# Optimization experiments

Hardware: AMD Instinct MI355X
Metric: run time of the kernel (lower is better)

## Reference

```python
import jax, jax.numpy as jnp
import numpy as np

MARGIN = 1.0


def setup_inputs() -> dict:
    key = jax.random.key(0)
    k1, k2 = jax.random.split(key)
    N, D, C = 8192, 128, 64
    embeddings = jax.random.normal(k1, (N, D), dtype=jnp.float32)
    labels = jax.random.randint(k2, (N,), 0, C, dtype=jnp.int64)
    return {"embeddings": embeddings, "labels": labels}


def _pairwise_euclidean(x):
    # ||xi - xj|| via Gram trick; safe sqrt (zero grad at 0, matches masked use)
    sq = jnp.sum(x * x, axis=1)                      # [N]
    d2 = sq[:, None] + sq[None, :] - 2.0 * (x @ x.T)  # [N, N]
    d2 = jnp.maximum(d2, 0.0)
    pos = d2 > 0.0
    return jnp.where(pos, jnp.sqrt(jnp.where(pos, d2, 1.0)), 0.0)


def reference(embeddings, labels):
    N = embeddings.shape[0]
    dist = _pairwise_euclidean(embeddings)            # [N, N]
    same = labels[:, None] == labels[None, :]         # [N, N]
    eye = jnp.eye(N, dtype=bool)
    pos_mask = same & ~eye
    neg_mask = ~same

    neg_inf = jnp.float32(-jnp.inf)
    pos_inf = jnp.float32(jnp.inf)
    hardest_pos = jnp.max(jnp.where(pos_mask, dist, neg_inf), axis=1)  # [N]
    hardest_neg = jnp.min(jnp.where(neg_mask, dist, pos_inf), axis=1)  # [N]

    has_pos = jnp.any(pos_mask, axis=1)
    has_neg = jnp.any(neg_mask, axis=1)
    tl = jax.nn.relu(hardest_pos - hardest_neg + MARGIN)               # [N]
    valid = has_pos & has_neg & (tl > 0.0)

    total = jnp.sum(jnp.where(valid, tl, 0.0))
    count = jnp.sum(valid)
    return jnp.where(count > 0, total / jnp.maximum(count, 1).astype(total.dtype), jnp.float32(0.0))
```

## Files before the change

### kernel.cpp

```cpp
#include <hip/hip_runtime.h>
#include <math.h>

#define NN 8192
#define DD 128
#define BM 256
#define BN 64
#define NPART 16
#define JRANGE (NN / NPART)
#define NTILES (JRANGE / BN)

typedef __attribute__((ext_vector_type(4))) int i32x4;

#define WS_SJC 0
#define WS_HPK (NN * 16)
#define WS_HNK (WS_HPK + NN * 4)
#define WS_AH  (WS_HNK + NN * 4)
#define WS_AL  (WS_AH + NN * DD)

__device__ __forceinline__ unsigned fkey(float f) {
    unsigned u = __float_as_uint(f);
    return (u & 0x80000000u) ? ~u : (u | 0x80000000u);
}
__device__ __forceinline__ float fkey_inv(unsigned k) {
    unsigned u = (k & 0x80000000u) ? (k ^ 0x80000000u) : ~k;
    return __uint_as_float(u);
}

__global__ __launch_bounds__(256)
void prepq_k(const float* __restrict__ emb, const int* __restrict__ lab,
             float4* __restrict__ sjc, unsigned* __restrict__ hpK,
             unsigned* __restrict__ hnK, int* __restrict__ aH, int* __restrict__ aL) {
    const int lane = threadIdx.x & 63;
    const int w    = threadIdx.x >> 6;
    const int half = lane >> 5;
    const int l32  = lane & 31;
    const int row  = blockIdx.x * 8 + w * 2 + half;

    float4 v = reinterpret_cast<const float4*>(emb)[row * 32 + l32];
    float s = 0.f, m = 0.f;
    s = fmaf(v.x, v.x, s); m = fmaxf(m, fabsf(v.x));
    s = fmaf(v.y, v.y, s); m = fmaxf(m, fabsf(v.y));
    s = fmaf(v.z, v.z, s); m = fmaxf(m, fabsf(v.z));
    s = fmaf(v.w, v.w, s); m = fmaxf(m, fabsf(v.w));
#pragma unroll
    for (int off = 1; off < 32; off <<= 1) {
        s += __shfl_xor(s, off, 64);
        m = fmaxf(m, __shfl_xor(m, off, 64));
    }
    m = fmaxf(m, 1e-30f);
    float sA  = m * (1.0f / 127.0f);
    float inv = 127.0f / m;
    int h = 0, l = 0;
#define QSTEP(X, K) { \
        float a = rintf((X) * inv); \
        a = fminf(fmaxf(a, -127.f), 127.f); \
        float r = fmaf(-a, sA, (X)); \
        float b = rintf(r * inv * 256.0f); \
        b = fminf(fmaxf(b, -127.f), 127.f); \
        h |= ((int)a & 255) << (8 * (K)); \
        l |= ((int)b & 255) << (8 * (K)); }
    QSTEP(v.x, 0) QSTEP(v.y, 1) QSTEP(v.z, 2) QSTEP(v.w, 3)
#undef QSTEP
    const int nidx = (row >> 4) * 512 + (l32 >> 4) * 256 + ((l32 >> 2) & 3) * 64
                   + (row & 15) * 4 + (l32 & 3);
    aH[nidx] = h;
    aL[nidx] = l;
    if (l32 == 0) {
        sjc[row] = make_float4(s, sA * 0.08838834764831845f,
                               __int_as_float(lab[row]), 0.f);
    }
    if (threadIdx.x < 8) {
        int r0 = blockIdx.x * 8 + threadIdx.x;
        hpK[r0] = 0x007FFFFFu;
        hnK[r0] = 0xFF800000u;
    }
}

__global__ __launch_bounds__(256, 2)
void hardest_k(const int* __restrict__ aH, const int* __restrict__ aL,
               const float4* __restrict__ sjc,
               unsigned* __restrict__ hpK, unsigned* __restrict__ hnK) {
    const int tid  = threadIdx.x;
    const int w    = tid >> 6;
    const int lane = tid & 63;
    const int lrow = lane & 15;
    const int lk   = lane >> 4;
    const int ib   = (int)blockIdx.x >> 4;
    const int part = (int)blockIdx.x & 15;
    const int i0   = ib * BM;
    const int jbeg = part * JRANGE;

    i32x4 ah[4][2], al[4][2];
#pragma unroll
    for (int s = 0; s < 4; ++s) {
        const int gA = ib * 16 + w * 4 + s;
#pragma unroll
        for (int q = 0; q < 2; ++q) {
            ah[s][q] = *reinterpret_cast<const i32x4*>(&aH[gA * 512 + q * 256 + lane * 4]);
            al[s][q] = *reinterpret_cast<const i32x4*>(&aL[gA * 512 + q * 256 + lane * 4]);
        }
    }
    int   li[4][4];
    float cih[4][4], hpg[4][4], hng[4][4];
#pragma unroll
    for (int s = 0; s < 4; ++s)
#pragma unroll
        for (int t = 0; t < 4; ++t) {
            float4 md = sjc[i0 + w * 64 + s * 16 + lk * 4 + t];
            li[s][t]  = __float_as_int(md.z);
            cih[s][t] = md.y;
            hpg[s][t] = -INFINITY;
            hng[s][t] =  INFINITY;
        }

#pragma unroll 1
    for (int jt = 0; jt < NTILES; ++jt) {
        const int j0 = jbeg + jt * BN;
#pragma unroll
        for (int c = 0; c < 4; ++c) {
            const int gB = (j0 >> 4) + c;
            const int bb = gB * 512 + lane * 4;
            i32x4 bh0 = *reinterpret_cast<const i32x4*>(&aH[bb]);
            i32x4 bh1 = *reinterpret_cast<const i32x4*>(&aH[bb + 256]);
            i32x4 bl0 = *reinterpret_cast<const i32x4*>(&aL[bb]);
            i32x4 bl1 = *reinterpret_cast<const i32x4*>(&aL[bb + 256]);
            float4 sv = sjc[j0 + c * 16 + lrow];
            i32x4 accA[4], accB[4];
            i32x4 zero = {0, 0, 0, 0};
#pragma unroll
            for (int s = 0; s < 4; ++s) { accA[s] = zero; accB[s] = zero; }
#pragma unroll
            for (int s = 0; s < 4; ++s) {
                accA[s] = __builtin_amdgcn_mfma_i32_16x16x64_i8(ah[s][0], bh0, accA[s], 0, 0, 0);
                accA[s] = __builtin_amdgcn_mfma_i32_16x16x64_i8(ah[s][1], bh1, accA[s], 0, 0, 0);
                accB[s] = __builtin_amdgcn_mfma_i32_16x16x64_i8(ah[s][0], bl0, accB[s], 0, 0, 0);
                accB[s] = __builtin_amdgcn_mfma_i32_16x16x64_i8(ah[s][1], bl1, accB[s], 0, 0, 0);
                accB[s] = __builtin_amdgcn_mfma_i32_16x16x64_i8(al[s][0], bh0, accB[s], 0, 0, 0);
                accB[s] = __builtin_amdgcn_mfma_i32_16x16x64_i8(al[s][1], bh1, accB[s], 0, 0, 0);
            }
            const float sqj = sv.x;
            const float cjv = sv.y;
            const int   lj  = __float_as_int(sv.z);
#pragma unroll
            for (int s = 0; s < 4; ++s)
#pragma unroll
                for (int t = 0; t < 4; ++t) {
                    int   e  = (accA[s][t] << 8) + accB[s][t];
                    float ef = (float)e;
                    float mm = cih[s][t] * cjv;
                    float gg = fmaf(mm, -ef, sqj);
                    bool same = (li[s][t] == lj);
                    hpg[s][t] = fmaxf(hpg[s][t], same ? gg : -INFINITY);
                    hng[s][t] = fminf(hng[s][t], same ? INFINITY : gg);
                }
        }
    }

#pragma unroll
    for (int off = 1; off < 16; off <<= 1)
#pragma unroll
        for (int s = 0; s < 4; ++s)
#pragma unroll
            for (int t = 0; t < 4; ++t) {
                hpg[s][t] = fmaxf(hpg[s][t], __shfl_xor(hpg[s][t], off, 64));
                hng[s][t] = fminf(hng[s][t], __shfl_xor(hng[s][t], off, 64));
            }
    if (lrow == 0) {
#pragma unroll
        for (int s = 0; s < 4; ++s)
#pragma unroll
            for (int t = 0; t < 4; ++t) {
                int i = i0 + w * 64 + s * 16 + lk * 4 + t;
                atomicMax(&hpK[i], fkey(hpg[s][t]));
                atomicMin(&hnK[i], fkey(hng[s][t]));
            }
    }
}

__global__ __launch_bounds__(1024)
void final_k(const unsigned* __restrict__ hpK, const unsigned* __restrict__ hnK,
             const float4* __restrict__ sjc, float* __restrict__ out) {
    float total = 0.f, cnt = 0.f;
    for (int i = threadIdx.x; i < NN; i += 1024) {
        float hp = fkey_inv(hpK[i]);
        float hn = fkey_inv(hnK[i]);
        float s  = sjc[i].x;
        float hp2 = s + hp, hn2 = s + hn;
        float hpd = (hp2 == -INFINITY) ? -INFINITY : sqrtf(fmaxf(hp2, 0.f));
        float hnd = (hn2 ==  INFINITY) ?  INFINITY : sqrtf(fmaxf(hn2, 0.f));
        float tl = hpd - hnd + 1.0f;
        if (tl > 0.f) { total += tl; cnt += 1.f; }
    }
#pragma unroll
    for (int off = 1; off < 64; off <<= 1) {
        total += __shfl_xor(total, off, 64);
        cnt   += __shfl_xor(cnt,   off, 64);
    }
    __shared__ float sT[16], sC[16];
    int wave = threadIdx.x >> 6;
    if ((threadIdx.x & 63) == 0) { sT[wave] = total; sC[wave] = cnt; }
    __syncthreads();
    if (threadIdx.x == 0) {
        float T = 0.f, Cn = 0.f;
#pragma unroll
        for (int k = 0; k < 16; ++k) { T += sT[k]; Cn += sC[k]; }
        out[0] = (Cn > 0.f) ? T / Cn : 0.f;
    }
}

extern "C" void kernel_launch(void* const* d_in, const int* in_sizes, int n_in,
                              void* d_out, int out_size, void* d_ws, size_t ws_size,
                              hipStream_t stream) {
    const float* emb = (const float*)d_in[0];
    const int*   lab = (const int*)d_in[1];
    char* ws = (char*)d_ws;
    float4*   sjc = (float4*)(ws + WS_SJC);
    unsigned* hpK = (unsigned*)(ws + WS_HPK);
    unsigned* hnK = (unsigned*)(ws + WS_HNK);
    int*      aH  = (int*)(ws + WS_AH);
    int*      aL  = (int*)(ws + WS_AL);

    prepq_k<<<dim3(NN / 8), dim3(256), 0, stream>>>(emb, lab, sjc, hpK, hnK, aH, aL);
    hardest_k<<<dim3((NN / BM) * NPART), dim3(256), 0, stream>>>(aH, aL, sjc, hpK, hnK);
    final_k<<<dim3(1), dim3(1024), 0, stream>>>(hpK, hnK, sjc, (float*)d_out);
}
```

Baseline: 48.30 us.

## Exploit distance-matrix symmetry by computing only upper-triangular block pairs

The hardest-mining kernel now launches one block per upper-triangular pair of 256-row super-blocks instead of sweeping all row/column tiles. Each computed dot-product tile updates both the row-wise hardest positive/negative and, through a column-wise reduction and atomics, the column-side extremes. This roughly halves the int8 MFMA work and the loads of B tiles. In exchange it adds per-element VALU work, cross-lane shuffles and many more global atomics per tile, and the serial loop that maps the block index to a triangular pair.

After: 59.46 us. +23.1%, slower.

```diff
diff --git a/kernel.cpp b/kernel.cpp
--- a/kernel.cpp
+++ b/kernel.cpp
@@ -3,11 +3,8 @@
 
 #define NN 8192
 #define DD 128
-#define BM 256
-#define BN 64
-#define NPART 16
-#define JRANGE (NN / NPART)
-#define NTILES (JRANGE / BN)
+#define NSB 32
+#define NBLK (NSB * (NSB + 1) / 2)
 
 typedef __attribute__((ext_vector_type(4))) int i32x4;
 
@@ -85,15 +82,17 @@
     const int lane = tid & 63;
     const int lrow = lane & 15;
     const int lk   = lane >> 4;
-    const int ib   = (int)blockIdx.x >> 4;
-    const int part = (int)blockIdx.x & 15;
-    const int i0   = ib * BM;
-    const int jbeg = part * JRANGE;
+
+    int rem = (int)blockIdx.x, bi = 0;
+    while (rem >= NSB - bi) { rem -= NSB - bi; ++bi; }
+    const int bj = bi + rem;
+    const int i0     = bi * 256;
+    const int j0base = bj * 256;
 
     i32x4 ah[4][2], al[4][2];
 #pragma unroll
     for (int s = 0; s < 4; ++s) {
-        const int gA = ib * 16 + w * 4 + s;
+        const int gA = bi * 16 + w * 4 + s;
 #pragma unroll
         for (int q = 0; q < 2; ++q) {
             ah[s][q] = *reinterpret_cast<const i32x4*>(&aH[gA * 512 + q * 256 + lane * 4]);
@@ -101,58 +100,68 @@
         }
     }
     int   li[4][4];
-    float cih[4][4], hpg[4][4], hng[4][4];
+    float cih[4][4], sqA[4][4], hpg[4][4], hng[4][4];
 #pragma unroll
     for (int s = 0; s < 4; ++s)
 #pragma unroll
         for (int t = 0; t < 4; ++t) {
-            float4 md = sjc[i0 + w * 64 + s * 16 + lk * 4 + t];
-            li[s][t]  = __float_as_int(md.z);
-            cih[s][t] = md.y;
+            float4 mdv = sjc[i0 + w * 64 + s * 16 + lk * 4 + t];
+            sqA[s][t] = mdv.x;
+            cih[s][t] = mdv.y;
+            li[s][t]  = __float_as_int(mdv.z);
             hpg[s][t] = -INFINITY;
             hng[s][t] =  INFINITY;
         }
 
 #pragma unroll 1
-    for (int jt = 0; jt < NTILES; ++jt) {
-        const int j0 = jbeg + jt * BN;
-#pragma unroll
-        for (int c = 0; c < 4; ++c) {
-            const int gB = (j0 >> 4) + c;
-            const int bb = gB * 512 + lane * 4;
-            i32x4 bh0 = *reinterpret_cast<const i32x4*>(&aH[bb]);
-            i32x4 bh1 = *reinterpret_cast<const i32x4*>(&aH[bb + 256]);
-            i32x4 bl0 = *reinterpret_cast<const i32x4*>(&aL[bb]);
-            i32x4 bl1 = *reinterpret_cast<const i32x4*>(&aL[bb + 256]);
-            float4 sv = sjc[j0 + c * 16 + lrow];
-            i32x4 accA[4], accB[4];
-            i32x4 zero = {0, 0, 0, 0};
-#pragma unroll
-            for (int s = 0; s < 4; ++s) { accA[s] = zero; accB[s] = zero; }
-#pragma unroll
-            for (int s = 0; s < 4; ++s) {
-                accA[s] = __builtin_amdgcn_mfma_i32_16x16x64_i8(ah[s][0], bh0, accA[s], 0, 0, 0);
-                accA[s] = __builtin_amdgcn_mfma_i32_16x16x64_i8(ah[s][1], bh1, accA[s], 0, 0, 0);
-                accB[s] = __builtin_amdgcn_mfma_i32_16x16x64_i8(ah[s][0], bl0, accB[s], 0, 0, 0);
-                accB[s] = __builtin_amdgcn_mfma_i32_16x16x64_i8(ah[s][1], bl1, accB[s], 0, 0, 0);
-                accB[s] = __builtin_amdgcn_mfma_i32_16x16x64_i8(al[s][0], bh0, accB[s], 0, 0, 0);
-                accB[s] = __builtin_amdgcn_mfma_i32_16x16x64_i8(al[s][1], bh1, accB[s], 0, 0, 0);
+    for (int c = 0; c < 16; ++c) {
+        const int gB = bj * 16 + c;
+        const int bb = gB * 512 + lane * 4;
+        i32x4 bh0 = *reinterpret_cast<const i32x4*>(&aH[bb]);
+        i32x4 bh1 = *reinterpret_cast<const i32x4*>(&aH[bb + 256]);
+        i32x4 bl0 = *reinterpret_cast<const i32x4*>(&aL[bb]);
+        i32x4 bl1 = *reinterpret_cast<const i32x4*>(&aL[bb + 256]);
+        float4 sv = sjc[j0base + c * 16 + lrow];
+        i32x4 accA[4], accB[4];
+        i32x4 zero = {0, 0, 0, 0};
+#pragma unroll
+        for (int s = 0; s < 4; ++s) { accA[s] = zero; accB[s] = zero; }
+#pragma unroll
+        for (int s = 0; s < 4; ++s) {
+            accA[s] = __builtin_amdgcn_mfma_i32_16x16x64_i8(ah[s][0], bh0, accA[s], 0, 0, 0);
+            accA[s] = __builtin_amdgcn_mfma_i32_16x16x64_i8(ah[s][1], bh1, accA[s], 0, 0, 0);
+            accB[s] = __builtin_amdgcn_mfma_i32_16x16x64_i8(ah[s][0], bl0, accB[s], 0, 0, 0);
+            accB[s] = __builtin_amdgcn_mfma_i32_16x16x64_i8(ah[s][1], bl1, accB[s], 0, 0, 0);
+            accB[s] = __builtin_amdgcn_mfma_i32_16x16x64_i8(al[s][0], bh0, accB[s], 0, 0, 0);
+            accB[s] = __builtin_amdgcn_mfma_i32_16x16x64_i8(al[s][1], bh1, accB[s], 0, 0, 0);
+        }
+        const float sqj = sv.x;
+        const float cjv = sv.y;
+        const int   lj  = __float_as_int(sv.z);
+        float cp = -INFINITY, cn = INFINITY;
+#pragma unroll
+        for (int s = 0; s < 4; ++s)
+#pragma unroll
+            for (int t = 0; t < 4; ++t) {
+                int   e  = (accA[s][t] << 8) + accB[s][t];
+                float ef = (float)e;
+                float mm = cih[s][t] * cjv;
+                float gg = fmaf(mm, -ef, sqj);
+                float vv = fmaf(mm, -ef, sqA[s][t]);
+                bool same = (li[s][t] == lj);
+                hpg[s][t] = fmaxf(hpg[s][t], same ? gg : -INFINITY);
+                hng[s][t] = fminf(hng[s][t], same ? INFINITY : gg);
+                cp = fmaxf(cp, same ? vv : -INFINITY);
+                cn = fminf(cn, same ? INFINITY : vv);
             }
-            const float sqj = sv.x;
-            const float cjv = sv.y;
-            const int   lj  = __float_as_int(sv.z);
-#pragma unroll
-            for (int s = 0; s < 4; ++s)
-#pragma unroll
-                for (int t = 0; t < 4; ++t) {
-                    int   e  = (accA[s][t] << 8) + accB[s][t];
-                    float ef = (float)e;
-                    float mm = cih[s][t] * cjv;
-                    float gg = fmaf(mm, -ef, sqj);
-                    bool same = (li[s][t] == lj);
-                    hpg[s][t] = fmaxf(hpg[s][t], same ? gg : -INFINITY);
-                    hng[s][t] = fminf(hng[s][t], same ? INFINITY : gg);
-                }
+        cp = fmaxf(cp, __shfl_xor(cp, 16, 64));
+        cp = fmaxf(cp, __shfl_xor(cp, 32, 64));
+        cn = fminf(cn, __shfl_xor(cn, 16, 64));
+        cn = fminf(cn, __shfl_xor(cn, 32, 64));
+        if (lk == 0) {
+            int j = j0base + c * 16 + lrow;
+            atomicMax(&hpK[j], fkey(cp));
+            atomicMin(&hnK[j], fkey(cn));
         }
     }
 
@@ -221,6 +230,6 @@
     int*      aL  = (int*)(ws + WS_AL);
 
     prepq_k<<<dim3(NN / 8), dim3(256), 0, stream>>>(emb, lab, sjc, hpK, hnK, aH, aL);
-    hardest_k<<<dim3((NN / BM) * NPART), dim3(256), 0, stream>>>(aH, aL, sjc, hpK, hnK);
+    hardest_k<<<dim3(NBLK), dim3(256), 0, stream>>>(aH, aL, sjc, hpK, hnK);
     final_k<<<dim3(1), dim3(1024), 0, stream>>>(hpK, hnK, sjc, (float*)d_out);
 }
```

## Replace two-level int8 quantized Gram with single bf16 MFMA pass

Applied to the files above, without the earlier changes.

Embeddings are now converted to bf16 in a fragment-friendly layout and the Gram tile is computed with bf16 16x16x32 MFMAs accumulating in fp32, replacing the hi/lo int8 split that needed six int8 MFMAs per subtile. This cuts matrix instruction count and removes per-row scale handling and integer recombination in the epilogue. It trades accuracy: bf16 inputs carry fewer mantissa bits than the two-level int8 scheme, which may perturb the selected hardest positives and negatives.

Result: faster. 41.18 us (-14.7%).

```diff
diff --git a/kernel.cpp b/kernel.cpp
--- a/kernel.cpp
+++ b/kernel.cpp
@@ -1,4 +1,5 @@
 #include <hip/hip_runtime.h>
+#include <hip/hip_bf16.h>
 #include <math.h>
 
 #define NN 8192
@@ -9,13 +10,13 @@
 #define JRANGE (NN / NPART)
 #define NTILES (JRANGE / BN)
 
-typedef __attribute__((ext_vector_type(4))) int i32x4;
+typedef __attribute__((ext_vector_type(8))) short bf16x8;
+typedef __attribute__((ext_vector_type(4))) float f32x4;
 
 #define WS_SJC 0
-#define WS_HPK (NN * 16)
+#define WS_HPK 65536
 #define WS_HNK (WS_HPK + NN * 4)
-#define WS_AH  (WS_HNK + NN * 4)
-#define WS_AL  (WS_AH + NN * DD)
+#define WS_AB  (WS_HNK + NN * 4)
 
 __device__ __forceinline__ unsigned fkey(float f) {
     unsigned u = __float_as_uint(f);
@@ -25,11 +26,15 @@
     unsigned u = (k & 0x80000000u) ? (k ^ 0x80000000u) : ~k;
     return __uint_as_float(u);
 }
+__device__ __forceinline__ ushort f2bf(float x) {
+    __hip_bfloat16 h = __float2bfloat16(x);
+    return *reinterpret_cast<ushort*>(&h);
+}
 
 __global__ __launch_bounds__(256)
 void prepq_k(const float* __restrict__ emb, const int* __restrict__ lab,
-             float4* __restrict__ sjc, unsigned* __restrict__ hpK,
-             unsigned* __restrict__ hnK, int* __restrict__ aH, int* __restrict__ aL) {
+             float2* __restrict__ sjc, unsigned* __restrict__ hpK,
+             unsigned* __restrict__ hnK, ushort* __restrict__ aB) {
     const int lane = threadIdx.x & 63;
     const int w    = threadIdx.x >> 6;
     const int half = lane >> 5;
@@ -37,38 +42,19 @@
     const int row  = blockIdx.x * 8 + w * 2 + half;
 
     float4 v = reinterpret_cast<const float4*>(emb)[row * 32 + l32];
-    float s = 0.f, m = 0.f;
-    s = fmaf(v.x, v.x, s); m = fmaxf(m, fabsf(v.x));
-    s = fmaf(v.y, v.y, s); m = fmaxf(m, fabsf(v.y));
-    s = fmaf(v.z, v.z, s); m = fmaxf(m, fabsf(v.z));
-    s = fmaf(v.w, v.w, s); m = fmaxf(m, fabsf(v.w));
-#pragma unroll
-    for (int off = 1; off < 32; off <<= 1) {
-        s += __shfl_xor(s, off, 64);
-        m = fmaxf(m, __shfl_xor(m, off, 64));
-    }
-    m = fmaxf(m, 1e-30f);
-    float sA  = m * (1.0f / 127.0f);
-    float inv = 127.0f / m;
-    int h = 0, l = 0;
-#define QSTEP(X, K) { \
-        float a = rintf((X) * inv); \
-        a = fminf(fmaxf(a, -127.f), 127.f); \
-        float r = fmaf(-a, sA, (X)); \
-        float b = rintf(r * inv * 256.0f); \
-        b = fminf(fmaxf(b, -127.f), 127.f); \
-        h |= ((int)a & 255) << (8 * (K)); \
-        l |= ((int)b & 255) << (8 * (K)); }
-    QSTEP(v.x, 0) QSTEP(v.y, 1) QSTEP(v.z, 2) QSTEP(v.w, 3)
-#undef QSTEP
-    const int nidx = (row >> 4) * 512 + (l32 >> 4) * 256 + ((l32 >> 2) & 3) * 64
-                   + (row & 15) * 4 + (l32 & 3);
-    aH[nidx] = h;
-    aL[nidx] = l;
-    if (l32 == 0) {
-        sjc[row] = make_float4(s, sA * 0.08838834764831845f,
-                               __int_as_float(lab[row]), 0.f);
-    }
+    float s = 0.f;
+    s = fmaf(v.x, v.x, s); s = fmaf(v.y, v.y, s);
+    s = fmaf(v.z, v.z, s); s = fmaf(v.w, v.w, s);
+#pragma unroll
+    for (int off = 1; off < 32; off <<= 1) s += __shfl_xor(s, off, 64);
+
+    ushort4 b;
+    b.x = f2bf(v.x); b.y = f2bf(v.y); b.z = f2bf(v.z); b.w = f2bf(v.w);
+    const int idx = (row >> 4) * 2048 + (l32 >> 3) * 512 + ((l32 >> 1) & 3) * 128
+                  + (row & 15) * 8 + (l32 & 1) * 4;
+    *reinterpret_cast<ushort4*>(aB + idx) = b;
+
+    if (l32 == 0) sjc[row] = make_float2(s, __int_as_float(lab[row]));
     if (threadIdx.x < 8) {
         int r0 = blockIdx.x * 8 + threadIdx.x;
         hpK[r0] = 0x007FFFFFu;
@@ -77,8 +63,7 @@
 }
 
 __global__ __launch_bounds__(256, 2)
-void hardest_k(const int* __restrict__ aH, const int* __restrict__ aL,
-               const float4* __restrict__ sjc,
+void hardest_k(const ushort* __restrict__ aB, const float2* __restrict__ sjc,
                unsigned* __restrict__ hpK, unsigned* __restrict__ hnK) {
     const int tid  = threadIdx.x;
     const int w    = tid >> 6;
@@ -90,25 +75,22 @@
     const int i0   = ib * BM;
     const int jbeg = part * JRANGE;
 
-    i32x4 ah[4][2], al[4][2];
+    bf16x8 a[4][4];
 #pragma unroll
     for (int s = 0; s < 4; ++s) {
         const int gA = ib * 16 + w * 4 + s;
 #pragma unroll
-        for (int q = 0; q < 2; ++q) {
-            ah[s][q] = *reinterpret_cast<const i32x4*>(&aH[gA * 512 + q * 256 + lane * 4]);
-            al[s][q] = *reinterpret_cast<const i32x4*>(&aL[gA * 512 + q * 256 + lane * 4]);
-        }
+        for (int q = 0; q < 4; ++q)
+            a[s][q] = *reinterpret_cast<const bf16x8*>(&aB[gA * 2048 + q * 512 + lane * 8]);
     }
     int   li[4][4];
-    float cih[4][4], hpg[4][4], hng[4][4];
+    float hpg[4][4], hng[4][4];
 #pragma unroll
     for (int s = 0; s < 4; ++s)
 #pragma unroll
         for (int t = 0; t < 4; ++t) {
-            float4 md = sjc[i0 + w * 64 + s * 16 + lk * 4 + t];
-            li[s][t]  = __float_as_int(md.z);
-            cih[s][t] = md.y;
+            float2 md = sjc[i0 + w * 64 + s * 16 + lk * 4 + t];
+            li[s][t]  = __float_as_int(md.y);
             hpg[s][t] = -INFINITY;
             hng[s][t] =  INFINITY;
         }
@@ -119,36 +101,30 @@
 #pragma unroll
         for (int c = 0; c < 4; ++c) {
             const int gB = (j0 >> 4) + c;
-            const int bb = gB * 512 + lane * 4;
-            i32x4 bh0 = *reinterpret_cast<const i32x4*>(&aH[bb]);
-            i32x4 bh1 = *reinterpret_cast<const i32x4*>(&aH[bb + 256]);
-            i32x4 bl0 = *reinterpret_cast<const i32x4*>(&aL[bb]);
-            i32x4 bl1 = *reinterpret_cast<const i32x4*>(&aL[bb + 256]);
-            float4 sv = sjc[j0 + c * 16 + lrow];
-            i32x4 accA[4], accB[4];
-            i32x4 zero = {0, 0, 0, 0};
-#pragma unroll
-            for (int s = 0; s < 4; ++s) { accA[s] = zero; accB[s] = zero; }
+            const ushort* bp = &aB[gB * 2048 + lane * 8];
+            bf16x8 b0 = *reinterpret_cast<const bf16x8*>(bp);
+            bf16x8 b1 = *reinterpret_cast<const bf16x8*>(bp + 512);
+            bf16x8 b2 = *reinterpret_cast<const bf16x8*>(bp + 1024);
+            bf16x8 b3 = *reinterpret_cast<const bf16x8*>(bp + 1536);
+            float2 sv = sjc[j0 + c * 16 + lrow];
+            f32x4 acc[4];
+            f32x4 zero = {0.f, 0.f, 0.f, 0.f};
+#pragma unroll
+            for (int s = 0; s < 4; ++s) acc[s] = zero;
 #pragma unroll
             for (int s = 0; s < 4; ++s) {
-                accA[s] = __builtin_amdgcn_mfma_i32_16x16x64_i8(ah[s][0], bh0, accA[s], 0, 0, 0);
-                accA[s] = __builtin_amdgcn_mfma_i32_16x16x64_i8(ah[s][1], bh1, accA[s], 0, 0, 0);
-                accB[s] = __builtin_amdgcn_mfma_i32_16x16x64_i8(ah[s][0], bl0, accB[s], 0, 0, 0);
-                accB[s] = __builtin_amdgcn_mfma_i32_16x16x64_i8(ah[s][1], bl1, accB[s], 0, 0, 0);
-                accB[s] = __builtin_amdgcn_mfma_i32_16x16x64_i8(al[s][0], bh0, accB[s], 0, 0, 0);
-                accB[s] = __builtin_amdgcn_mfma_i32_16x16x64_i8(al[s][1], bh1, accB[s], 0, 0, 0);
+                acc[s] = __builtin_amdgcn_mfma_f32_16x16x32_bf16(a[s][0], b0, acc[s], 0, 0, 0);
+                acc[s] = __builtin_amdgcn_mfma_f32_16x16x32_bf16(a[s][1], b1, acc[s], 0, 0, 0);
+                acc[s] = __builtin_amdgcn_mfma_f32_16x16x32_bf16(a[s][2], b2, acc[s], 0, 0, 0);
+                acc[s] = __builtin_amdgcn_mfma_f32_16x16x32_bf16(a[s][3], b3, acc[s], 0, 0, 0);
             }
             const float sqj = sv.x;
-            const float cjv = sv.y;
-            const int   lj  = __float_as_int(sv.z);
+            const int   lj  = __float_as_int(sv.y);
 #pragma unroll
             for (int s = 0; s < 4; ++s)
 #pragma unroll
                 for (int t = 0; t < 4; ++t) {
-                    int   e  = (accA[s][t] << 8) + accB[s][t];
-                    float ef = (float)e;
-                    float mm = cih[s][t] * cjv;
-                    float gg = fmaf(mm, -ef, sqj);
+                    float gg = fmaf(-2.f, acc[s][t], sqj);
                     bool same = (li[s][t] == lj);
                     hpg[s][t] = fmaxf(hpg[s][t], same ? gg : -INFINITY);
                     hng[s][t] = fminf(hng[s][t], same ? INFINITY : gg);
@@ -179,7 +155,7 @@
 
 __global__ __launch_bounds__(1024)
 void final_k(const unsigned* __restrict__ hpK, const unsigned* __restrict__ hnK,
-             const float4* __restrict__ sjc, float* __restrict__ out) {
+             const float2* __restrict__ sjc, float* __restrict__ out) {
     float total = 0.f, cnt = 0.f;
     for (int i = threadIdx.x; i < NN; i += 1024) {
         float hp = fkey_inv(hpK[i]);
@@ -214,13 +190,12 @@
     const float* emb = (const float*)d_in[0];
     const int*   lab = (const int*)d_in[1];
     char* ws = (char*)d_ws;
-    float4*   sjc = (float4*)(ws + WS_SJC);
+    float2*   sjc = (float2*)(ws + WS_SJC);
     unsigned* hpK = (unsigned*)(ws + WS_HPK);
     unsigned* hnK = (unsigned*)(ws + WS_HNK);
-    int*      aH  = (int*)(ws + WS_AH);
-    int*      aL  = (int*)(ws + WS_AL);
-
-    prepq_k<<<dim3(NN / 8), dim3(256), 0, stream>>>(emb, lab, sjc, hpK, hnK, aH, aL);
-    hardest_k<<<dim3((NN / BM) * NPART), dim3(256), 0, stream>>>(aH, aL, sjc, hpK, hnK);
+    ushort*   aB  = (ushort*)(ws + WS_AB);
+
+    prepq_k<<<dim3(NN / 8), dim3(256), 0, stream>>>(emb, lab, sjc, hpK, hnK, aB);
+    hardest_k<<<dim3((NN / BM) * NPART), dim3(256), 0, stream>>>(aB, sjc, hpK, hnK);
     final_k<<<dim3(1), dim3(1024), 0, stream>>>(hpK, hnK, sjc, (float*)d_out);
 }
```
